# Optimization experiments

Measured on AMD Instinct MI355X. Metric: run time of the kernel, lower is better.

The kernel has to match this reference:

```python
import jax, jax.numpy as jnp
import numpy as np

OFR = 2.0      # offset_range_factor
WSIZE = 8      # window_size
SPLIT = 1      # split_size


def _grid_sample(img, grid):
    # torch.nn.functional.grid_sample: bilinear, align_corners=True, padding_mode='zeros'
    # img: (B,C,H,W); grid: (B,Gh,Gw,2) with (x,y) in [-1,1]
    B, C, H, W = img.shape
    gx = (grid[..., 0] + 1.0) * 0.5 * (W - 1)
    gy = (grid[..., 1] + 1.0) * 0.5 * (H - 1)
    x0 = jnp.floor(gx)
    y0 = jnp.floor(gy)
    wx1 = gx - x0
    wy1 = gy - y0
    imgf = img.reshape(B, C, H * W)

    def corner(yc, xc, wgt):
        valid = (xc >= 0) & (xc <= W - 1) & (yc >= 0) & (yc <= H - 1)
        idx = (jnp.clip(yc, 0, H - 1) * W + jnp.clip(xc, 0, W - 1)).astype(jnp.int32)
        g = jnp.take_along_axis(imgf, idx.reshape(B, 1, -1), axis=2)  # (B,C,N)
        return g * (wgt * valid).reshape(B, 1, -1)

    out = (corner(y0, x0, (1 - wy1) * (1 - wx1)) + corner(y0, x0 + 1, (1 - wy1) * wx1)
           + corner(y0 + 1, x0, wy1 * (1 - wx1)) + corner(y0 + 1, x0 + 1, wy1 * wx1))
    return out.reshape(B, C, *grid.shape[1:-1])


def _win_attn(xqv, dh, dw):
    # 'b (qv c) (h dh) (w dw) -> qv (b h w) (dh dw) c' ; dot attention ; inverse rearrange
    B, cc, H, W = xqv.shape
    c = cc // 2
    t = xqv.reshape(B, 2, c, H // dh, dh, W // dw, dw)
    t = t.transpose(1, 0, 3, 5, 4, 6, 2).reshape(2, -1, dh * dw, c)
    q, v = t[0], t[1]
    atn = jax.nn.softmax(q @ jnp.swapaxes(q, -1, -2), axis=-1)
    o = atn @ v  # (nw, dh*dw, c)
    o = o.reshape(B, H // dh, W // dw, dh, dw, c).transpose(0, 5, 1, 3, 2, 4).reshape(B, c, H, W)
    return o


def setup_inputs() -> dict:
    key = jax.random.key(0)
    ks = jax.random.split(key, 16)
    C, B, H, W = 48, 2, 64, 64
    rn = lambda k, s, sc=0.05: (jax.random.normal(k, s) * sc).astype(jnp.float32)
    return {
        'x': jax.random.normal(ks[0], (B, C, H, W), jnp.float32),
        'Wq': rn(ks[1], (C, C)), 'bq': rn(ks[2], (C,)),
        'off_dw_w': rn(ks[3], (C, 1, 3, 3)), 'off_dw_b': rn(ks[4], (C,)),
        'off_ln_g': jnp.ones((C,), jnp.float32), 'off_ln_b': jnp.zeros((C,), jnp.float32),
        'off_pw_w': rn(ks[5], (2, C)),
        'Wk': rn(ks[6], (C, C)), 'bk': rn(ks[7], (C,)),
        'Wv': rn(ks[8], (C, C)), 'bv': rn(ks[9], (C,)),
        'inp_w': rn(ks[10], (2 * C, C)), 'inp_b': rn(ks[11], (2 * C,)),
        'bn_g': jnp.ones((2 * C,), jnp.float32), 'bn_b': jnp.zeros((2 * C,), jnp.float32),
        'bn_mean': jnp.zeros((2 * C,), jnp.float32), 'bn_var': jnp.ones((2 * C,), jnp.float32),
        'pout_w': rn(ks[12], (C, C)), 'pout_b': rn(ks[13], (C,)),
        'rpe': rn(ks[14], (1, 191, 191), 0.01),  # 96*2-1
    }


def reference(x, Wq, bq, off_dw_w, off_dw_b, off_ln_g, off_ln_b, off_pw_w, Wk, bk, Wv, bv,
              inp_w, inp_b, bn_g, bn_b, bn_mean, bn_var, pout_w, pout_b, rpe):
    B, C, h, w = x.shape
    scale = C ** (-0.5)
    c1 = lambda t, W_, b_=None: jnp.einsum('oc,bchw->bohw', W_, t) + (0.0 if b_ is None else b_[None, :, None, None])
    q = c1(x, Wq, bq)
    # conv_offset: depthwise 3x3 -> LayerNorm over channels -> GELU -> 1x1 to 2 ch (no bias)
    t = jax.lax.conv_general_dilated(q, off_dw_w, (1, 1), ((1, 1), (1, 1)),
                                     dimension_numbers=('NCHW', 'OIHW', 'NCHW'),
                                     feature_group_count=C) + off_dw_b[None, :, None, None]
    mu = t.mean(1, keepdims=True)
    var = ((t - mu) ** 2).mean(1, keepdims=True)
    t = (t - mu) * jax.lax.rsqrt(var + 1e-5) * off_ln_g[None, :, None, None] + off_ln_b[None, :, None, None]
    t = jax.nn.gelu(t, approximate=False)
    offset = c1(t, off_pw_w)  # (B,2,h,w), channel 0 = y, 1 = x
    n = h * w
    orange = jnp.array([1.0 / (h - 1), 1.0 / (w - 1)], jnp.float32).reshape(1, 2, 1, 1)
    offset = jnp.tanh(offset) * orange * OFR
    offset = offset.transpose(0, 2, 3, 1)  # (B,h,w,2) (y,x)
    ry = jnp.linspace(0.5, h - 0.5, h) / (h - 1) * 2.0 - 1.0
    rx = jnp.linspace(0.5, w - 0.5, w) / (w - 1) * 2.0 - 1.0
    ref = jnp.stack(jnp.meshgrid(ry, rx, indexing='ij'), -1)[None]
    pos = offset + ref  # (B,h,w,2) (y,x)
    x_sampled = _grid_sample(x, pos[..., ::-1]).reshape(B, C, n)
    # project_inp: 1x1 conv -> BatchNorm2d (eval mode)
    x2 = c1(x, inp_w, inp_b)
    x2 = (x2 - bn_mean[None, :, None, None]) * jax.lax.rsqrt(bn_var + 1e-5)[None, :, None, None] \
         * bn_g[None, :, None, None] + bn_b[None, :, None, None]
    s = 2 * C // 3
    xs0, xs1, xs2 = x2[:, :s], x2[:, s:2 * s], x2[:, 2 * s:]
    # deformable global attention
    qf = q.reshape(B, C, n)
    k = jnp.einsum('oc,bcn->bon', Wk, x_sampled) + bk[None, :, None]
    v = jnp.einsum('oc,bcn->bon', Wv, x_sampled) + bv[None, :, None]
    attn = jnp.einsum('bcm,bcn->bmn', qf, k) * scale
    gy = jnp.arange(h, dtype=jnp.float32) / (h - 1) * 2.0 - 1.0
    gx = jnp.arange(w, dtype=jnp.float32) / (w - 1) * 2.0 - 1.0
    qg = jnp.stack(jnp.meshgrid(gy, gx, indexing='ij'), -1).reshape(n, 2)
    disp = (qg[None, :, None, :] - pos.reshape(B, n, 2)[:, None, :, :]) * 0.5  # (B,m,n,2) (y,x)
    rpe_img = jnp.broadcast_to(rpe[None], (B,) + rpe.shape)  # (B,1,191,191)
    attn_bias = _grid_sample(rpe_img, disp[..., ::-1]).reshape(B, n, n)
    attn = jax.nn.softmax(attn + attn_bias, axis=2)
    out_dat = jnp.einsum('bmn,bcn->bcm', attn, v).reshape(B, C, h, w)
    # windowed / column / row local attention (shifts=0)
    out = jnp.concatenate([_win_attn(xs0, WSIZE, WSIZE),
                           _win_attn(xs1, h, SPLIT),
                           _win_attn(xs2, SPLIT, w)], axis=1)
    out = c1(out, pout_w, pout_b)
    return out * 0.5 + out_dat * 0.5
```

## Files before the change

kernel.cpp:

```cpp
#include <hip/hip_runtime.h>
#include <hip/hip_bf16.h>
#include <math.h>

#define Bsz 2
#define Cch 48
#define Hh 64
#define Ww 64
#define Nn 4096

typedef __bf16 bf16;
typedef __attribute__((ext_vector_type(8))) __bf16 bf16x8;
typedef __attribute__((ext_vector_type(4))) float f32x4;

__global__ void k_conv1x1(const float* __restrict__ in, const float* __restrict__ Wt,
                          const float* __restrict__ bias, float* __restrict__ qnc,
                          bf16* __restrict__ qbf){
  int chunk = blockIdx.x & 15;
  int o = (blockIdx.x >> 4) % Cch;
  int b = blockIdx.x / (16 * Cch);
  int p = chunk * 256 + threadIdx.x;
  float acc = bias[o];
  const float* ip = in + (b * Cch) * Nn + p;
  const float* wp = Wt + o * Cch;
  #pragma unroll
  for (int c = 0; c < Cch; c++) acc += wp[c] * ip[c * Nn];
  qnc[((size_t)(b * Nn + p)) * 48 + o] = acc;
  size_t qb = ((size_t)(b * Nn + p)) * 64;
  qbf[qb + o] = (bf16)acc;
  if (o < 16) qbf[qb + 48 + o] = (bf16)0.f;
}

__global__ __launch_bounds__(256) void k_offset_pos(const float* __restrict__ qnc,
                             const float* __restrict__ dww,
                             const float* __restrict__ dwb, const float* __restrict__ lng,
                             const float* __restrict__ lnb, const float* __restrict__ pww,
                             float* __restrict__ pos){
  int wv = threadIdx.x >> 6, lane = threadIdx.x & 63;
  int idx = blockIdx.x * 4 + wv;
  int b = idx >> 12;
  int p = idx & (Nn - 1);
  int y = p >> 6, x = p & 63;
  int c = lane;
  float t = 0.f;
  if (c < 48){
    t = dwb[c];
    #pragma unroll
    for (int ky = -1; ky <= 1; ky++){
      int yy = y + ky;
      if (yy < 0 || yy >= Hh) continue;
      #pragma unroll
      for (int kx = -1; kx <= 1; kx++){
        int xx = x + kx;
        if (xx < 0 || xx >= Ww) continue;
        t = fmaf(qnc[((size_t)(b * Nn + yy * Ww + xx)) * 48 + c],
                 dww[c * 9 + (ky + 1) * 3 + (kx + 1)], t);
      }
    }
  }
  float s = t;
  #pragma unroll
  for (int m = 1; m < 64; m <<= 1) s += __shfl_xor(s, m);
  float mean = s * (1.f / 48.f);
  float d = (c < 48) ? (t - mean) : 0.f;
  float v = d * d;
  #pragma unroll
  for (int m = 1; m < 64; m <<= 1) v += __shfl_xor(v, m);
  float rstd = rsqrtf(v * (1.f / 48.f) + 1e-5f);
  float p0 = 0.f, p1 = 0.f;
  if (c < 48){
    float u = (t - mean) * rstd * lng[c] + lnb[c];
    u = 0.5f * u * (1.f + erff(u * 0.70710678118654752f));
    p0 = pww[c] * u;
    p1 = pww[48 + c] * u;
  }
  #pragma unroll
  for (int m = 1; m < 64; m <<= 1){ p0 += __shfl_xor(p0, m); p1 += __shfl_xor(p1, m); }
  if (lane == 0){
    float posy = tanhf(p0) * (2.f / 63.f) + ((0.5f + (float)y) * (2.f / 63.f) - 1.f);
    float posx = tanhf(p1) * (2.f / 63.f) + ((0.5f + (float)x) * (2.f / 63.f) - 1.f);
    pos[idx * 2 + 0] = posy;
    pos[idx * 2 + 1] = posx;
  }
}

__global__ __launch_bounds__(512) void k_samplekv(const float* __restrict__ x,
                           const float* __restrict__ pos,
                           const float* __restrict__ Wk, const float* __restrict__ bk,
                           const float* __restrict__ Wv, const float* __restrict__ bv,
                           bf16* __restrict__ kk_bf, bf16* __restrict__ vt_bf,
                           float2* __restrict__ axay){
  __shared__ float wkt[48][49];
  __shared__ float wvt[48][49];
  __shared__ float rowb[8][48];
  int tid = threadIdx.x;
  for (int f = tid; f < 2304; f += 512){
    int o = f / 48, c = f - o * 48;
    wkt[c][o] = Wk[f];
    wvt[c][o] = Wv[f];
  }
  __syncthreads();
  int wv = tid >> 6, lane = tid & 63;
  int idx = blockIdx.x * 8 + wv;
  int b = idx >> 12;
  int n = idx & (Nn - 1);
  float py = pos[idx * 2], px = pos[idx * 2 + 1];
  if (lane == 0) axay[idx] = make_float2(95.f - 47.5f * py, 95.f - 47.5f * px);
  float gx = (px + 1.f) * 0.5f * 63.f;
  float gy = (py + 1.f) * 0.5f * 63.f;
  float x0f = floorf(gx), y0f = floorf(gy);
  float wx = gx - x0f, wy = gy - y0f;
  int x0 = (int)x0f, y0 = (int)y0f, x1 = x0 + 1, y1 = y0 + 1;
  float w00 = (1.f - wy) * (1.f - wx), w01 = (1.f - wy) * wx;
  float w10 = wy * (1.f - wx),         w11 = wy * wx;
  bool vx0 = (x0 >= 0) && (x0 < Ww), vx1 = (x1 >= 0) && (x1 < Ww);
  bool vy0 = (y0 >= 0) && (y0 < Hh), vy1 = (y1 >= 0) && (y1 < Hh);
  if (!(vx0 && vy0)) w00 = 0.f;
  if (!(vx1 && vy0)) w01 = 0.f;
  if (!(vx0 && vy1)) w10 = 0.f;
  if (!(vx1 && vy1)) w11 = 0.f;
  int cx0 = min(max(x0, 0), Ww - 1), cx1 = min(max(x1, 0), Ww - 1);
  int cy0 = min(max(y0, 0), Hh - 1), cy1 = min(max(y1, 0), Hh - 1);
  int i00 = cy0 * Ww + cx0, i01 = cy0 * Ww + cx1;
  int i10 = cy1 * Ww + cx0, i11 = cy1 * Ww + cx1;
  int c = lane;
  if (c < 48){
    const float* xc = x + ((size_t)(b * Cch + c)) * Nn;
    rowb[wv][c] = w00 * xc[i00] + w01 * xc[i01] + w10 * xc[i10] + w11 * xc[i11];
  }
  int o = lane;
  if (o < 48){
    float ka = bk[o], va = bv[o];
    #pragma unroll
    for (int cc = 0; cc < 48; cc++){
      float r = rowb[wv][cc];
      ka = fmaf(wkt[cc][o], r, ka);
      va = fmaf(wvt[cc][o], r, va);
    }
    kk_bf[(size_t)idx * 64 + o] = (bf16)ka;
    vt_bf[((size_t)(b * Cch + o)) * Nn + n] = (bf16)va;
  }
  if (o < 16) kk_bf[(size_t)idx * 64 + 48 + o] = (bf16)0.f;
}

__global__ __launch_bounds__(256, 5) void k_attn_win(const bf16* __restrict__ q_bf,
                                              const bf16* __restrict__ kk_bf,
                                              const bf16* __restrict__ vt_bf,
                                              const float2* __restrict__ axay,
                                              const float* __restrict__ rpe,
                                              float* __restrict__ o_part,
                                              float* __restrict__ s_part,
                                              const float* __restrict__ x,
                                              const float* __restrict__ iw,
                                              const float* __restrict__ ib,
                                              const float* __restrict__ bng,
                                              const float* __restrict__ bnb,
                                              const float* __restrict__ bnm,
                                              const float* __restrict__ bnv,
                                              float* __restrict__ wout){
  __shared__ __align__(16) char smem[25600];
  const int tid = threadIdx.x;
  const int wid = tid >> 6, lane = tid & 63;
  const int q16 = lane >> 4, l16 = lane & 15;

  if (blockIdx.x < 1024){
    float (*g)[26] = (float(*)[26])smem;
    float* axs  = (float*)(smem + 13312);
    int*   xlos = (int*)  (smem + 13824);
    float* wy0s = (float*)(smem + 14336);
    float* wy1s = (float*)(smem + 14848);
    int*   r0s  = (int*)  (smem + 15360);
    int*   r1s  = (int*)  (smem + 15872);
    bf16 (*ps)[136] = (bf16(*)[136])(smem + 16384);

    const int b  = blockIdx.x >> 9;
    const int kp = (blockIdx.x >> 8) & 1;
    const int m0 = (blockIdx.x & 255) * 16;
    const int wn0 = wid * 32;

    const bf16* qb = q_bf + ((size_t)(b * Nn + m0 + l16)) * 64;
    bf16x8 qf0 = *(const bf16x8*)(qb + q16 * 8);
    bf16x8 qf1 = *(const bf16x8*)(qb + 32 + q16 * 8);

    const float qgy = (float)(m0 >> 6) * (2.f / 63.f) - 1.f;
    const float byq = 47.5f * qgy;
    const float scale = 0.14433756729740643f;
    const float bx0 = 47.5f * ((float)(m0 & 63) * (2.f / 63.f) - 1.f);
    float bxr[4];
    #pragma unroll
    for (int r = 0; r < 4; r++){
      int mcol = (m0 & 63) + q16 * 4 + r;
      bxr[r] = 47.5f * ((float)mcol * (2.f / 63.f) - 1.f);
    }

    f32x4 oacc[3];
    #pragma unroll
    for (int ct = 0; ct < 3; ct++) oacc[ct] = (f32x4){0.f, 0.f, 0.f, 0.f};
    float s_runw[4] = {0.f, 0.f, 0.f, 0.f};

    for (int chk = 0; chk < 16; chk++){
      const int n0 = kp * 2048 + chk * 128;
      if (lane < 32){
        int n = wn0 + lane;
        float2 aa = axay[(size_t)b * Nn + n0 + n];
        float gyr = aa.x + byq;
        float y0f = floorf(gyr);
        float wy = gyr - y0f;
        int y0 = (int)y0f, y1 = y0 + 1;
        wy0s[n] = ((unsigned)y0 < 191u) ? (1.f - wy) : 0.f;
        wy1s[n] = ((unsigned)y1 < 191u) ? wy : 0.f;
        r0s[n] = min(max(y0, 0), 190) * 191;
        r1s[n] = min(max(y1, 0), 190) * 191;
        axs[n] = aa.y;
        xlos[n] = (int)floorf(aa.y + bx0);
      }
      {
        int s = lane >> 5, jj = lane & 31;
        if (jj < 26){
          #pragma unroll
          for (int it = 0; it < 16; it++){
            int n = wn0 + it * 2 + s;
            int xg = xlos[n] + jj;
            int cx = min(max(xg, 0), 190);
            float val = wy0s[n] * rpe[r0s[n] + cx] + wy1s[n] * rpe[r1s[n] + cx];
            g[n][jj] = ((unsigned)xg < 191u) ? val : 0.f;
          }
        }
      }
      f32x4 s0 = (f32x4){0.f, 0.f, 0.f, 0.f};
      f32x4 s1 = (f32x4){0.f, 0.f, 0.f, 0.f};
      {
        const bf16* kg = kk_bf + (size_t)(b * Nn + n0 + wn0 + l16) * 64;
        bf16x8 b00 = *(const bf16x8*)(kg + q16 * 8);
        bf16x8 b01 = *(const bf16x8*)(kg + 32 + q16 * 8);
        bf16x8 b10 = *(const bf16x8*)(kg + 16 * 64 + q16 * 8);
        bf16x8 b11 = *(const bf16x8*)(kg + 16 * 64 + 32 + q16 * 8);
        s0 = __builtin_amdgcn_mfma_f32_16x16x32_bf16(qf0, b00, s0, 0, 0, 0);
        s0 = __builtin_amdgcn_mfma_f32_16x16x32_bf16(qf1, b01, s0, 0, 0, 0);
        s1 = __builtin_amdgcn_mfma_f32_16x16x32_bf16(qf0, b10, s1, 0, 0, 0);
        s1 = __builtin_amdgcn_mfma_f32_16x16x32_bf16(qf1, b11, s1, 0, 0, 0);
      }
      #pragma unroll
      for (int nt = 0; nt < 2; nt++){
        int nl = wn0 + nt * 16 + l16;
        float ax = axs[nl];
        int xb = xlos[nl];
        f32x4 sv = nt ? s1 : s0;
        #pragma unroll
        for (int r = 0; r < 4; r++){
          float gxr = ax + bxr[r];
          float x0f = floorf(gxr);
          float wx = gxr - x0f;
          int j0 = (int)x0f - xb;
          float g0 = g[nl][j0], g1 = g[nl][j0 + 1];
          float bias = fmaf(wx, g1 - g0, g0);
          float e = __expf(fmaf(sv[r], scale, bias));
          s_runw[r] += e;
          ps[q16 * 4 + r][nl] = (bf16)e;
        }
      }
      {
        bf16x8 pa = *(const bf16x8*)&ps[l16][wn0 + q16 * 8];
        const bf16* vgb = vt_bf + (size_t)(b * Cch + l16) * Nn + n0 + wn0 + q16 * 8;
        #pragma unroll
        for (int ct = 0; ct < 3; ct++){
          bf16x8 vb = *(const bf16x8*)(vgb + (size_t)(ct * 16) * Nn);
          oacc[ct] = __builtin_amdgcn_mfma_f32_16x16x32_bf16(pa, vb, oacc[ct], 0, 0, 0);
        }
      }
    }
    #pragma unroll
    for (int r = 0; r < 4; r++){
      #pragma unroll
      for (int msk = 1; msk < 16; msk <<= 1)
        s_runw[r] += __shfl_xor(s_runw[r], msk);
    }
    __syncthreads();
    float* ored = (float*)g;
    float* sred = axs;
    #pragma unroll
    for (int ct = 0; ct < 3; ct++)
      #pragma unroll
      for (int r = 0; r < 4; r++)
        ored[(wid * 16 + q16 * 4 + r) * 48 + ct * 16 + l16] = oacc[ct][r];
    if (l16 == 0){
      #pragma unroll
      for (int r = 0; r < 4; r++) sred[wid * 16 + q16 * 4 + r] = s_runw[r];
    }
    __syncthreads();
    size_t obase = ((size_t)(b * 2 + kp) * Cch) * Nn;
    #pragma unroll
    for (int e = 0; e < 3; e++){
      int idx = tid + e * 256;
      int c = idx >> 4, mm = idx & 15;
      float v = ored[mm * 48 + c] + ored[(16 + mm) * 48 + c]
              + ored[(32 + mm) * 48 + c] + ored[(48 + mm) * 48 + c];
      o_part[obase + (size_t)c * Nn + m0 + mm] = v;
    }
    if (tid < 16)
      s_part[(size_t)(b * 2 + kp) * Nn + m0 + tid] =
          sred[tid] + sred[16 + tid] + sred[32 + tid] + sred[48 + tid];
  } else {
    bf16 (*xs)[72]  = (bf16(*)[72])smem;
    bf16 (*wtt)[72] = (bf16(*)[72])(smem + 9216);
    bf16 (*qs)[72]  = (bf16(*)[72])(smem + 13824);
    bf16 (*vst)[72] = (bf16(*)[72])(smem + 23040);
    float* bnsc = (float*)(smem + 25344);
    float* bnsh = (float*)(smem + 25472);
    bf16 (*psw)[72] = xs;

    int wb = blockIdx.x - 1024;
    int s = wb >> 7;
    int r7 = wb & 127;
    int b = r7 >> 6, wi = r7 & 63;
    for (int f = tid; f < 64 * 48; f += 256){
      int t = f & 63, c = f >> 6;
      int p = (s == 0) ? (((wi >> 3) * 8 + (t >> 3)) * 64 + (wi & 7) * 8 + (t & 7))
            : (s == 1) ? (t * 64 + wi) : (wi * 64 + t);
      xs[t][c] = (bf16)x[((size_t)(b * 48 + c)) * Nn + p];
    }
    for (int f = tid; f < 64 * 16; f += 256){
      int t = f >> 4, j = f & 15;
      xs[t][48 + j] = (bf16)0.f;
      qs[t][16 + j] = (bf16)0.f;
    }
    for (int f = tid; f < 32 * 64; f += 256){
      int o = f >> 6, c = f & 63;
      wtt[o][c] = (c < 48) ? (bf16)iw[(s * 32 + o) * 48 + c] : (bf16)0.f;
    }
    if (tid < 32){
      int ch = s * 32 + tid;
      float sc = bng[ch] * rsqrtf(bnv[ch] + 1e-5f);
      bnsc[tid] = sc;
      bnsh[tid] = (ib[ch] - bnm[ch]) * sc + bnb[ch];
    }
    __syncthreads();
    {
      bf16x8 a0 = *(const bf16x8*)&xs[wid * 16 + l16][q16 * 8];
      bf16x8 a1 = *(const bf16x8*)&xs[wid * 16 + l16][32 + q16 * 8];
      #pragma unroll
      for (int nt = 0; nt < 2; nt++){
        bf16x8 b0 = *(const bf16x8*)&wtt[nt * 16 + l16][q16 * 8];
        bf16x8 b1 = *(const bf16x8*)&wtt[nt * 16 + l16][32 + q16 * 8];
        f32x4 acc = (f32x4){0.f, 0.f, 0.f, 0.f};
        acc = __builtin_amdgcn_mfma_f32_16x16x32_bf16(a0, b0, acc, 0, 0, 0);
        acc = __builtin_amdgcn_mfma_f32_16x16x32_bf16(a1, b1, acc, 0, 0, 0);
        float scv = bnsc[nt * 16 + l16], shv = bnsh[nt * 16 + l16];
        #pragma unroll
        for (int r = 0; r < 4; r++){
          float v = fmaf(acc[r], scv, shv);
          int tok = wid * 16 + q16 * 4 + r;
          if (nt == 0) qs[tok][l16] = (bf16)v;
          else         vst[l16][tok] = (bf16)v;
        }
      }
    }
    __syncthreads();
    f32x4 sreg[4];
    {
      bf16x8 aq = *(const bf16x8*)&qs[wid * 16 + l16][q16 * 8];
      #pragma unroll
      for (int nt = 0; nt < 4; nt++){
        bf16x8 bq = *(const bf16x8*)&qs[nt * 16 + l16][q16 * 8];
        f32x4 acc = (f32x4){0.f, 0.f, 0.f, 0.f};
        sreg[nt] = __builtin_amdgcn_mfma_f32_16x16x32_bf16(aq, bq, acc, 0, 0, 0);
      }
    }
    float rinv[4];
    #pragma unroll
    for (int r = 0; r < 4; r++){
      float mx = fmaxf(fmaxf(sreg[0][r], sreg[1][r]), fmaxf(sreg[2][r], sreg[3][r]));
      #pragma unroll
      for (int msk = 1; msk < 16; msk <<= 1) mx = fmaxf(mx, __shfl_xor(mx, msk));
      float sum = 0.f;
      #pragma unroll
      for (int nt = 0; nt < 4; nt++){
        float e = __expf(sreg[nt][r] - mx);
        sum += e;
        psw[wid * 16 + q16 * 4 + r][nt * 16 + l16] = (bf16)e;
      }
      #pragma unroll
      for (int msk = 1; msk < 16; msk <<= 1) sum += __shfl_xor(sum, msk);
      rinv[r] = 1.f / sum;
    }
    f32x4 oac = (f32x4){0.f, 0.f, 0.f, 0.f};
    {
      bf16x8 pa0 = *(const bf16x8*)&psw[wid * 16 + l16][q16 * 8];
      bf16x8 pa1 = *(const bf16x8*)&psw[wid * 16 + l16][32 + q16 * 8];
      bf16x8 vb0 = *(const bf16x8*)&vst[l16][q16 * 8];
      bf16x8 vb1 = *(const bf16x8*)&vst[l16][32 + q16 * 8];
      oac = __builtin_amdgcn_mfma_f32_16x16x32_bf16(pa0, vb0, oac, 0, 0, 0);
      oac = __builtin_amdgcn_mfma_f32_16x16x32_bf16(pa1, vb1, oac, 0, 0, 0);
    }
    #pragma unroll
    for (int r = 0; r < 4; r++){
      int tok = wid * 16 + q16 * 4 + r;
      int p = (s == 0) ? (((wi >> 3) * 8 + (tok >> 3)) * 64 + (wi & 7) * 8 + (tok & 7))
            : (s == 1) ? (tok * 64 + wi) : (wi * 64 + tok);
      wout[((size_t)(b * 48 + s * 16 + l16)) * Nn + p] = oac[r] * rinv[r];
    }
  }
}

__global__ void k_final(const float* __restrict__ win, const float* __restrict__ pw,
                        const float* __restrict__ pb, const float* __restrict__ o_part,
                        const float* __restrict__ s_part, float* __restrict__ out){
  int chunk = blockIdx.x & 15;
  int o = (blockIdx.x >> 4) % Cch;
  int b = blockIdx.x / (16 * Cch);
  int p = chunk * 256 + threadIdx.x;
  float acc = pb[o];
  const float* ip = win + (b * Cch) * Nn + p;
  const float* wp = pw + o * Cch;
  #pragma unroll
  for (int c = 0; c < Cch; c++) acc += wp[c] * ip[c * Nn];
  float sden = s_part[(size_t)(b * 2) * Nn + p] + s_part[(size_t)(b * 2 + 1) * Nn + p];
  float odv = (o_part[((size_t)(b * 2) * Cch + o) * Nn + p]
             + o_part[((size_t)(b * 2 + 1) * Cch + o) * Nn + p]) / sden;
  out[(b * Cch + o) * Nn + p] = 0.5f * acc + 0.5f * odv;
}

extern "C" void kernel_launch(void* const* d_in, const int* in_sizes, int n_in,
                              void* d_out, int out_size, void* d_ws, size_t ws_size,
                              hipStream_t stream){
  const float* x   = (const float*)d_in[0];
  const float* Wq  = (const float*)d_in[1];
  const float* bq  = (const float*)d_in[2];
  const float* dww = (const float*)d_in[3];
  const float* dwb = (const float*)d_in[4];
  const float* lng = (const float*)d_in[5];
  const float* lnb = (const float*)d_in[6];
  const float* pww = (const float*)d_in[7];
  const float* Wk  = (const float*)d_in[8];
  const float* bk  = (const float*)d_in[9];
  const float* Wv  = (const float*)d_in[10];
  const float* bv  = (const float*)d_in[11];
  const float* iw  = (const float*)d_in[12];
  const float* ib  = (const float*)d_in[13];
  const float* bng = (const float*)d_in[14];
  const float* bnb = (const float*)d_in[15];
  const float* bnm = (const float*)d_in[16];
  const float* bnv = (const float*)d_in[17];
  const float* pw  = (const float*)d_in[18];
  const float* pb  = (const float*)d_in[19];
  const float* rpe = (const float*)d_in[20];

  float*  ws     = (float*)d_ws;
  float*  qnc    = ws;
  float*  o_part = ws;
  float*  pos    = ws + 786432;
  float2* axay   = (float2*)(ws + 802816);
  float*  wout   = ws + 819200;
  bf16*   q_bf   = (bf16*)(ws + 1212416);
  bf16*   kk_bf  = (bf16*)(ws + 1474560);
  bf16*   vt_bf  = (bf16*)(ws + 1736704);
  float*  s_part = ws + 1933312;
  float*  out    = (float*)d_out;

  k_conv1x1   <<<Bsz * Cch * 16, 256, 0, stream>>>(x, Wq, bq, qnc, q_bf);
  k_offset_pos<<<(Bsz * Nn) / 4, 256, 0, stream>>>(qnc, dww, dwb, lng, lnb, pww, pos);
  k_samplekv  <<<(Bsz * Nn) / 8, 512, 0, stream>>>(x, pos, Wk, bk, Wv, bv,
                                                   kk_bf, vt_bf, axay);
  k_attn_win  <<<Bsz * 512 + 384, 256, 0, stream>>>(q_bf, kk_bf, vt_bf, axay, rpe,
                                                    o_part, s_part,
                                                    x, iw, ib, bng, bnb, bnm, bnv, wout);
  k_final     <<<Bsz * Cch * 16, 256, 0, stream>>>(wout, pw, pb, o_part,
                                                   s_part, out);
}
```

Baseline: 199.3 us.

## Process 32 queries per attention block to reuse K/V loads and RPE tiles

Doubles the query tile per attention block from 16 to 32 rows, so each loaded K and V fragment and each interpolated RPE bias row tile is shared by two MFMA query subtiles. The bias gather tile widens from 26 to 50 columns to cover the wider query span, and the grid halves its attention blocks. This cuts redundant global K/V traffic and rpe gathers per query, at the cost of more shared memory and registers and lower occupancy (launch bounds 5 down to 4) with fewer blocks.

New measurement: 201.2 us. About the same (+1.0%).

```diff
diff --git a/kernel.cpp b/kernel.cpp
--- a/kernel.cpp
+++ b/kernel.cpp
@@ -142,7 +142,7 @@
   if (o < 16) kk_bf[(size_t)idx * 64 + 48 + o] = (bf16)0.f;
 }
 
-__global__ __launch_bounds__(256, 5) void k_attn_win(const bf16* __restrict__ q_bf,
+__global__ __launch_bounds__(256, 4) void k_attn_win(const bf16* __restrict__ q_bf,
                                               const bf16* __restrict__ kk_bf,
                                               const bf16* __restrict__ vt_bf,
                                               const float2* __restrict__ axay,
@@ -157,45 +157,51 @@
                                               const float* __restrict__ bnm,
                                               const float* __restrict__ bnv,
                                               float* __restrict__ wout){
-  __shared__ __align__(16) char smem[25600];
+  __shared__ __align__(16) char smem[37376];
   const int tid = threadIdx.x;
   const int wid = tid >> 6, lane = tid & 63;
   const int q16 = lane >> 4, l16 = lane & 15;
 
-  if (blockIdx.x < 1024){
-    float (*g)[26] = (float(*)[26])smem;
-    float* axs  = (float*)(smem + 13312);
-    int*   xlos = (int*)  (smem + 13824);
-    float* wy0s = (float*)(smem + 14336);
-    float* wy1s = (float*)(smem + 14848);
-    int*   r0s  = (int*)  (smem + 15360);
-    int*   r1s  = (int*)  (smem + 15872);
-    bf16 (*ps)[136] = (bf16(*)[136])(smem + 16384);
-
-    const int b  = blockIdx.x >> 9;
-    const int kp = (blockIdx.x >> 8) & 1;
-    const int m0 = (blockIdx.x & 255) * 16;
+  if (blockIdx.x < 512){
+    float (*g)[50] = (float(*)[50])smem;
+    float* axs  = (float*)(smem + 25600);
+    int*   xlos = (int*)  (smem + 26112);
+    float* wy0s = (float*)(smem + 26624);
+    float* wy1s = (float*)(smem + 27136);
+    int*   r0s  = (int*)  (smem + 27648);
+    int*   r1s  = (int*)  (smem + 28160);
+    bf16 (*ps)[136] = (bf16(*)[136])(smem + 28672);
+
+    const int b  = blockIdx.x >> 8;
+    const int kp = (blockIdx.x >> 7) & 1;
+    const int m0 = (blockIdx.x & 127) * 32;
     const int wn0 = wid * 32;
 
-    const bf16* qb = q_bf + ((size_t)(b * Nn + m0 + l16)) * 64;
-    bf16x8 qf0 = *(const bf16x8*)(qb + q16 * 8);
-    bf16x8 qf1 = *(const bf16x8*)(qb + 32 + q16 * 8);
+    bf16x8 qf0[2], qf1[2];
+    #pragma unroll
+    for (int qt = 0; qt < 2; qt++){
+      const bf16* qb = q_bf + ((size_t)(b * Nn + m0 + qt * 16 + l16)) * 64;
+      qf0[qt] = *(const bf16x8*)(qb + q16 * 8);
+      qf1[qt] = *(const bf16x8*)(qb + 32 + q16 * 8);
+    }
 
     const float qgy = (float)(m0 >> 6) * (2.f / 63.f) - 1.f;
     const float byq = 47.5f * qgy;
     const float scale = 0.14433756729740643f;
     const float bx0 = 47.5f * ((float)(m0 & 63) * (2.f / 63.f) - 1.f);
-    float bxr[4];
-    #pragma unroll
-    for (int r = 0; r < 4; r++){
-      int mcol = (m0 & 63) + q16 * 4 + r;
+    float bxr[8];
+    #pragma unroll
+    for (int r = 0; r < 8; r++){
+      int mcol = (m0 & 63) + (r >> 2) * 16 + q16 * 4 + (r & 3);
       bxr[r] = 47.5f * ((float)mcol * (2.f / 63.f) - 1.f);
     }
 
-    f32x4 oacc[3];
-    #pragma unroll
-    for (int ct = 0; ct < 3; ct++) oacc[ct] = (f32x4){0.f, 0.f, 0.f, 0.f};
-    float s_runw[4] = {0.f, 0.f, 0.f, 0.f};
+    f32x4 oacc[2][3];
+    #pragma unroll
+    for (int qt = 0; qt < 2; qt++)
+      #pragma unroll
+      for (int ct = 0; ct < 3; ct++) oacc[qt][ct] = (f32x4){0.f, 0.f, 0.f, 0.f};
+    float s_runw[8] = {0.f, 0.f, 0.f, 0.f, 0.f, 0.f, 0.f, 0.f};
 
     for (int chk = 0; chk < 16; chk++){
       const int n0 = kp * 2048 + chk * 128;
@@ -214,11 +220,11 @@
         xlos[n] = (int)floorf(aa.y + bx0);
       }
       {
-        int s = lane >> 5, jj = lane & 31;
-        if (jj < 26){
+        int jj = lane;
+        if (jj < 50){
           #pragma unroll
-          for (int it = 0; it < 16; it++){
-            int n = wn0 + it * 2 + s;
+          for (int it = 0; it < 32; it++){
+            int n = wn0 + it;
             int xg = xlos[n] + jj;
             int cx = min(max(xg, 0), 190);
             float val = wy0s[n] * rpe[r0s[n] + cx] + wy1s[n] * rpe[r1s[n] + cx];
@@ -226,50 +232,63 @@
           }
         }
       }
-      f32x4 s0 = (f32x4){0.f, 0.f, 0.f, 0.f};
-      f32x4 s1 = (f32x4){0.f, 0.f, 0.f, 0.f};
+      f32x4 sacc[2][2];
       {
         const bf16* kg = kk_bf + (size_t)(b * Nn + n0 + wn0 + l16) * 64;
         bf16x8 b00 = *(const bf16x8*)(kg + q16 * 8);
         bf16x8 b01 = *(const bf16x8*)(kg + 32 + q16 * 8);
         bf16x8 b10 = *(const bf16x8*)(kg + 16 * 64 + q16 * 8);
         bf16x8 b11 = *(const bf16x8*)(kg + 16 * 64 + 32 + q16 * 8);
-        s0 = __builtin_amdgcn_mfma_f32_16x16x32_bf16(qf0, b00, s0, 0, 0, 0);
-        s0 = __builtin_amdgcn_mfma_f32_16x16x32_bf16(qf1, b01, s0, 0, 0, 0);
-        s1 = __builtin_amdgcn_mfma_f32_16x16x32_bf16(qf0, b10, s1, 0, 0, 0);
-        s1 = __builtin_amdgcn_mfma_f32_16x16x32_bf16(qf1, b11, s1, 0, 0, 0);
-      }
-      #pragma unroll
-      for (int nt = 0; nt < 2; nt++){
-        int nl = wn0 + nt * 16 + l16;
-        float ax = axs[nl];
-        int xb = xlos[nl];
-        f32x4 sv = nt ? s1 : s0;
         #pragma unroll
-        for (int r = 0; r < 4; r++){
-          float gxr = ax + bxr[r];
-          float x0f = floorf(gxr);
-          float wx = gxr - x0f;
-          int j0 = (int)x0f - xb;
-          float g0 = g[nl][j0], g1 = g[nl][j0 + 1];
-          float bias = fmaf(wx, g1 - g0, g0);
-          float e = __expf(fmaf(sv[r], scale, bias));
-          s_runw[r] += e;
-          ps[q16 * 4 + r][nl] = (bf16)e;
+        for (int qt = 0; qt < 2; qt++){
+          f32x4 s0 = (f32x4){0.f, 0.f, 0.f, 0.f};
+          f32x4 s1 = (f32x4){0.f, 0.f, 0.f, 0.f};
+          s0 = __builtin_amdgcn_mfma_f32_16x16x32_bf16(qf0[qt], b00, s0, 0, 0, 0);
+          s0 = __builtin_amdgcn_mfma_f32_16x16x32_bf16(qf1[qt], b01, s0, 0, 0, 0);
+          s1 = __builtin_amdgcn_mfma_f32_16x16x32_bf16(qf0[qt], b10, s1, 0, 0, 0);
+          s1 = __builtin_amdgcn_mfma_f32_16x16x32_bf16(qf1[qt], b11, s1, 0, 0, 0);
+          sacc[qt][0] = s0;
+          sacc[qt][1] = s1;
         }
       }
+      #pragma unroll
+      for (int qt = 0; qt < 2; qt++){
+        #pragma unroll
+        for (int nt = 0; nt < 2; nt++){
+          int nl = wn0 + nt * 16 + l16;
+          float ax = axs[nl];
+          int xb = xlos[nl];
+          f32x4 sv = sacc[qt][nt];
+          #pragma unroll
+          for (int r = 0; r < 4; r++){
+            float gxr = ax + bxr[qt * 4 + r];
+            float x0f = floorf(gxr);
+            float wx = gxr - x0f;
+            int j0 = (int)x0f - xb;
+            float g0 = g[nl][j0], g1 = g[nl][j0 + 1];
+            float bias = fmaf(wx, g1 - g0, g0);
+            float e = __expf(fmaf(sv[r], scale, bias));
+            s_runw[qt * 4 + r] += e;
+            ps[qt * 16 + q16 * 4 + r][nl] = (bf16)e;
+          }
+        }
+      }
       {
-        bf16x8 pa = *(const bf16x8*)&ps[l16][wn0 + q16 * 8];
         const bf16* vgb = vt_bf + (size_t)(b * Cch + l16) * Nn + n0 + wn0 + q16 * 8;
+        bf16x8 vb0 = *(const bf16x8*)(vgb);
+        bf16x8 vb1 = *(const bf16x8*)(vgb + (size_t)16 * Nn);
+        bf16x8 vb2 = *(const bf16x8*)(vgb + (size_t)32 * Nn);
         #pragma unroll
-        for (int ct = 0; ct < 3; ct++){
-          bf16x8 vb = *(const bf16x8*)(vgb + (size_t)(ct * 16) * Nn);
-          oacc[ct] = __builtin_amdgcn_mfma_f32_16x16x32_bf16(pa, vb, oacc[ct], 0, 0, 0);
+        for (int qt = 0; qt < 2; qt++){
+          bf16x8 pa = *(const bf16x8*)&ps[qt * 16 + l16][wn0 + q16 * 8];
+          oacc[qt][0] = __builtin_amdgcn_mfma_f32_16x16x32_bf16(pa, vb0, oacc[qt][0], 0, 0, 0);
+          oacc[qt][1] = __builtin_amdgcn_mfma_f32_16x16x32_bf16(pa, vb1, oacc[qt][1], 0, 0, 0);
+          oacc[qt][2] = __builtin_amdgcn_mfma_f32_16x16x32_bf16(pa, vb2, oacc[qt][2], 0, 0, 0);
         }
       }
     }
     #pragma unroll
-    for (int r = 0; r < 4; r++){
+    for (int r = 0; r < 8; r++){
       #pragma unroll
       for (int msk = 1; msk < 16; msk <<= 1)
         s_runw[r] += __shfl_xor(s_runw[r], msk);
@@ -278,27 +297,30 @@
     float* ored = (float*)g;
     float* sred = axs;
     #pragma unroll
-    for (int ct = 0; ct < 3; ct++)
-      #pragma unroll
-      for (int r = 0; r < 4; r++)
-        ored[(wid * 16 + q16 * 4 + r) * 48 + ct * 16 + l16] = oacc[ct][r];
+    for (int qt = 0; qt < 2; qt++)
+      #pragma unroll
+      for (int ct = 0; ct < 3; ct++)
+        #pragma unroll
+        for (int r = 0; r < 4; r++)
+          ored[(wid * 32 + qt * 16 + q16 * 4 + r) * 48 + ct * 16 + l16] = oacc[qt][ct][r];
     if (l16 == 0){
       #pragma unroll
-      for (int r = 0; r < 4; r++) sred[wid * 16 + q16 * 4 + r] = s_runw[r];
+      for (int r = 0; r < 8; r++)
+        sred[wid * 32 + (r >> 2) * 16 + q16 * 4 + (r & 3)] = s_runw[r];
     }
     __syncthreads();
     size_t obase = ((size_t)(b * 2 + kp) * Cch) * Nn;
     #pragma unroll
-    for (int e = 0; e < 3; e++){
+    for (int e = 0; e < 6; e++){
       int idx = tid + e * 256;
-      int c = idx >> 4, mm = idx & 15;
-      float v = ored[mm * 48 + c] + ored[(16 + mm) * 48 + c]
-              + ored[(32 + mm) * 48 + c] + ored[(48 + mm) * 48 + c];
+      int c = idx >> 5, mm = idx & 31;
+      float v = ored[mm * 48 + c] + ored[(32 + mm) * 48 + c]
+              + ored[(64 + mm) * 48 + c] + ored[(96 + mm) * 48 + c];
       o_part[obase + (size_t)c * Nn + m0 + mm] = v;
     }
-    if (tid < 16)
+    if (tid < 32)
       s_part[(size_t)(b * 2 + kp) * Nn + m0 + tid] =
-          sred[tid] + sred[16 + tid] + sred[32 + tid] + sred[48 + tid];
+          sred[tid] + sred[32 + tid] + sred[64 + tid] + sred[96 + tid];
   } else {
     bf16 (*xs)[72]  = (bf16(*)[72])smem;
     bf16 (*wtt)[72] = (bf16(*)[72])(smem + 9216);
@@ -308,7 +330,7 @@
     float* bnsh = (float*)(smem + 25472);
     bf16 (*psw)[72] = xs;
 
-    int wb = blockIdx.x - 1024;
+    int wb = blockIdx.x - 512;
     int s = wb >> 7;
     int r7 = wb & 127;
     int b = r7 >> 6, wi = r7 & 63;
@@ -460,7 +482,7 @@
   k_offset_pos<<<(Bsz * Nn) / 4, 256, 0, stream>>>(qnc, dww, dwb, lng, lnb, pww, pos);
   k_samplekv  <<<(Bsz * Nn) / 8, 512, 0, stream>>>(x, pos, Wk, bk, Wv, bv,
                                                    kk_bf, vt_bf, axay);
-  k_attn_win  <<<Bsz * 512 + 384, 256, 0, stream>>>(q_bf, kk_bf, vt_bf, axay, rpe,
+  k_attn_win  <<<Bsz * 256 + 384, 256, 0, stream>>>(q_bf, kk_bf, vt_bf, axay, rpe,
                                                     o_part, s_part,
                                                     x, iw, ib, bng, bnb, bnm, bnv, wout);
   k_final     <<<Bsz * Cch * 16, 256, 0, stream>>>(wout, pw, pb, o_part,
```
